# Kernel tuning notes

Measured on AMD Instinct MI355X. Metric: run time of the kernel, lower is better.

Reference implementation:

```python
import jax, jax.numpy as jnp
import numpy as np

N, C = 50000, 91
K_PRE = 1000            # pre-NMS top-k candidates (fixed shape for jit)
DET_PER_IMG = 100
SCORE_THRESH = 0.05
NMS_THRESH = 0.5
MIN_SIZE = 0.01
LOG_SCALE_CLAMP = float(np.log(1000.0 / 16.0))  # torchvision BoxCoder clamp
BBOX_W = (10.0, 10.0, 5.0, 5.0)


def setup_inputs() -> dict:
    key = jax.random.key(0)
    k1, k2, k3, k4, k5, k6 = jax.random.split(key, 6)
    class_logits = jax.random.normal(k1, (N, C), jnp.float32) * 2.0
    box_regression = jax.random.normal(k2, (N, C * 4), jnp.float32) * 0.5
    x1 = jax.random.uniform(k3, (N,), jnp.float32) * 1200.0
    y1 = jax.random.uniform(k4, (N,), jnp.float32) * 700.0
    w = jax.random.uniform(k5, (N,), jnp.float32) * 150.0 + 4.0
    h = jax.random.uniform(k6, (N,), jnp.float32) * 150.0 + 4.0
    proposals = jnp.stack([x1, y1, x1 + w, y1 + h], axis=1)
    return {"class_logits": class_logits, "box_regression": box_regression,
            "proposals": proposals, "image_h": 800, "image_w": 1333}


def _decode(rel, props):
    # torchvision BoxCoder.decode_single with weights (10,10,5,5)
    wx, wy, ww, wh = BBOX_W
    pw = props[:, 2] - props[:, 0]
    ph = props[:, 3] - props[:, 1]
    cx = props[:, 0] + 0.5 * pw
    cy = props[:, 1] + 0.5 * ph
    dx = rel[:, 0] / wx
    dy = rel[:, 1] / wy
    dw = jnp.minimum(rel[:, 2] / ww, LOG_SCALE_CLAMP)
    dh = jnp.minimum(rel[:, 3] / wh, LOG_SCALE_CLAMP)
    pcx = dx * pw + cx
    pcy = dy * ph + cy
    ppw = jnp.exp(dw) * pw
    pph = jnp.exp(dh) * ph
    return jnp.stack([pcx - 0.5 * ppw, pcy - 0.5 * pph,
                      pcx + 0.5 * ppw, pcy + 0.5 * pph], axis=1)


def _iou_matrix(b):
    # b: [K,4] -> [K,K] pairwise IoU
    area = jnp.maximum(b[:, 2] - b[:, 0], 0.0) * jnp.maximum(b[:, 3] - b[:, 1], 0.0)
    lt = jnp.maximum(b[:, None, :2], b[None, :, :2])
    rb = jnp.minimum(b[:, None, 2:], b[None, :, 2:])
    wh = jnp.maximum(rb - lt, 0.0)
    inter = wh[..., 0] * wh[..., 1]
    return inter / (area[:, None] + area[None, :] - inter + 1e-7)


def _postprocess(class_logits, box_regression, proposals, image_h, image_w):
    num_classes = class_logits.shape[-1]
    n = proposals.shape[0]
    props = jnp.broadcast_to(proposals[:, None, :], (n, num_classes, 4)).reshape(-1, 4)
    boxes = _decode(box_regression.reshape(-1, 4), props)       # [N*C, 4]
    # clip_boxes_to_image
    boxes = jnp.stack([
        jnp.clip(boxes[:, 0], 0.0, float(image_w)),
        jnp.clip(boxes[:, 1], 0.0, float(image_h)),
        jnp.clip(boxes[:, 2], 0.0, float(image_w)),
        jnp.clip(boxes[:, 3], 0.0, float(image_h)),
    ], axis=1)
    scores = jax.nn.softmax(class_logits, axis=-1)               # [N, C]
    # drop background class 0
    boxes = boxes.reshape(n, num_classes, 4)[:, 1:].reshape(-1, 4)    # [N*(C-1), 4]
    scores = scores[:, 1:].reshape(-1)                                # [N*(C-1)]
    labels = jnp.broadcast_to(jnp.arange(1, num_classes), (n, num_classes - 1)).reshape(-1)
    # score threshold + remove small boxes -> mask (fixed-shape)
    w = boxes[:, 2] - boxes[:, 0]
    h = boxes[:, 3] - boxes[:, 1]
    valid = (scores > SCORE_THRESH) & (w >= MIN_SIZE) & (h >= MIN_SIZE)
    masked_scores = jnp.where(valid, scores, -1.0)
    s_k, idx = jax.lax.top_k(masked_scores, K_PRE)               # pre-NMS candidates
    b_k = boxes[idx]
    l_k = labels[idx]
    keep0 = s_k > 0.0
    # batched NMS via per-class coordinate offset
    offset = l_k.astype(b_k.dtype) * float(image_w + image_h + 2)
    iou = _iou_matrix(b_k + offset[:, None])                     # [K,K]
    ar = jnp.arange(K_PRE)
    def body(i, keep):
        sup = keep[i] & (iou[i] > NMS_THRESH) & (ar > i)
        return keep & ~sup
    keep = jax.lax.fori_loop(0, K_PRE, body, keep0)
    final_scores = jnp.where(keep, s_k, -1.0)
    s_out, j = jax.lax.top_k(final_scores, DET_PER_IMG)
    ok = s_out > 0.0
    boxes_out = jnp.where(ok[:, None], b_k[j], 0.0)
    scores_out = jnp.where(ok, s_out, 0.0)
    labels_out = jnp.where(ok, l_k[j], 0)
    return boxes_out, scores_out, labels_out


def reference(class_logits, box_regression, proposals, image_h, image_w):
    return _postprocess(class_logits, box_regression, proposals, image_h, image_w)
```

## Files before the change

### kernel.cpp

```cpp
#include <hip/hip_runtime.h>
#include <cstdint>

#define NROWS 50000
#define NCLS  91
#define KPRE  1000
#define NDET  100
#define CAP   4096
#define NBINS 512
#define BIN_OFF 7680u
#define LOGCLAMP 4.135166556742356f
#define ROWS_PER_BLOCK 16
#define P1BLK 3125
#define GCHUNK 128

constexpr size_t OFF_CNT     = 0;
constexpr size_t OFF_ROWMAX  = 64;
constexpr size_t OFF_COMPACT = 100096;
constexpr size_t OFF_SSCORE  = 132864;
constexpr size_t OFF_SGIDX   = 136960;
constexpr size_t OFF_SLABEL  = 141056;
constexpr size_t OFF_BRAW    = 145152;
constexpr size_t OFF_BNMS    = 161536;
constexpr size_t OFF_MASK    = 177920;

__device__ __forceinline__ bool decode_box(int row, int c,
    const float* __restrict__ regr, const float* __restrict__ props,
    float W, float H, float4& b) {
  const float4 rr = *reinterpret_cast<const float4*>(regr + (size_t)row * (NCLS * 4) + c * 4);
  const float4 pp = *reinterpret_cast<const float4*>(props + (size_t)row * 4);
  float pw = pp.z - pp.x, ph = pp.w - pp.y;
  float cx = pp.x + 0.5f * pw, cy = pp.y + 0.5f * ph;
  float dx = rr.x / 10.0f, dy = rr.y / 10.0f;
  float dw = fminf(rr.z / 5.0f, LOGCLAMP);
  float dh = fminf(rr.w / 5.0f, LOGCLAMP);
  float pcx = dx * pw + cx, pcy = dy * ph + cy;
  float ppw = expf(dw) * pw, pph = expf(dh) * ph;
  float x1 = fminf(fmaxf(pcx - 0.5f * ppw, 0.f), W);
  float y1 = fminf(fmaxf(pcy - 0.5f * pph, 0.f), H);
  float x2 = fminf(fmaxf(pcx + 0.5f * ppw, 0.f), W);
  float y2 = fminf(fmaxf(pcy + 0.5f * pph, 0.f), H);
  b = make_float4(x1, y1, x2, y2);
  return (x2 - x1 >= 0.01f) && (y2 - y1 >= 0.01f);
}

__global__ __launch_bounds__(256)
void pass1_kernel(const float* __restrict__ logits,
                  const float* __restrict__ regr,
                  const float* __restrict__ props,
                  const int* __restrict__ p_imh,
                  const int* __restrict__ p_imw,
                  uint16_t* __restrict__ rowmax) {
  const int gt  = blockIdx.x * 256 + threadIdx.x;
  const int row = gt >> 4;
  const int sub = gt & 15;
  const float* lr = logits + (size_t)row * NCLS;

  float x[6];
  #pragma unroll
  for (int j = 0; j < 6; ++j) {
    int c = sub + 16 * j;
    x[j] = (c < NCLS) ? lr[c] : -INFINITY;
  }
  float m = x[0];
  #pragma unroll
  for (int j = 1; j < 6; ++j) m = fmaxf(m, x[j]);
  m = fmaxf(m, __shfl_xor(m, 1));
  m = fmaxf(m, __shfl_xor(m, 2));
  m = fmaxf(m, __shfl_xor(m, 4));
  m = fmaxf(m, __shfl_xor(m, 8));
  float e[6]; float s = 0.f;
  #pragma unroll
  for (int j = 0; j < 6; ++j) {
    e[j] = (sub + 16 * j < NCLS) ? expf(x[j] - m) : 0.f;
    s += e[j];
  }
  s += __shfl_xor(s, 1);
  s += __shfl_xor(s, 2);
  s += __shfl_xor(s, 4);
  s += __shfl_xor(s, 8);

  const float W = (float)(*p_imw), H = (float)(*p_imh);
  int maxbin = 0;
  #pragma unroll
  for (int j = 0; j < 6; ++j) {
    int c = sub + 16 * j;
    if (c >= 1 && c < NCLS) {
      float score = e[j] / s;
      if (score > 0.05f) {
        float4 b;
        if (decode_box(row, c, regr, props, W, H, b)) {
          uint32_t bin = (__float_as_uint(score) >> 17) - BIN_OFF;
          if ((int)bin > maxbin) maxbin = (int)bin;
        }
      }
    }
  }
  maxbin = max(maxbin, __shfl_xor(maxbin, 1));
  maxbin = max(maxbin, __shfl_xor(maxbin, 2));
  maxbin = max(maxbin, __shfl_xor(maxbin, 4));
  maxbin = max(maxbin, __shfl_xor(maxbin, 8));
  if (sub == 0) rowmax[row] = (uint16_t)maxbin;
}

__global__ __launch_bounds__(512)
void histscan_kernel(const uint16_t* __restrict__ rowmax, uint32_t* __restrict__ cnt) {
  __shared__ uint32_t sh[NBINS];
  const int t = threadIdx.x;
  sh[t] = 0;
  if (t == 0) cnt[1] = 0;
  __syncthreads();
  const uint32_t* r32 = reinterpret_cast<const uint32_t*>(rowmax);
  for (int k = t; k < NROWS / 2; k += 512) {
    uint32_t v = r32[k];
    uint32_t a = v & 0xffffu, b = v >> 16;
    if (a) atomicAdd(&sh[a], 1u);
    if (b) atomicAdd(&sh[b], 1u);
  }
  __syncthreads();
  uint32_t v = sh[t];
  for (int off = 1; off < NBINS; off <<= 1) {
    uint32_t add = (t + off < NBINS) ? sh[t + off] : 0;
    __syncthreads();
    v += add;
    sh[t] = v;
    __syncthreads();
  }
  const uint32_t total = sh[0];
  if (total == 0) { if (t == 0) cnt[0] = 0xFFFFFFFFu; return; }
  const uint32_t target = total < (uint32_t)KPRE ? total : (uint32_t)KPRE;
  const uint32_t rs_t = sh[t];
  const uint32_t rs_n = (t < NBINS - 1) ? sh[t + 1] : 0;
  if (rs_t >= target && rs_n < target) cnt[0] = (uint32_t)t;
}

__global__ __launch_bounds__(256)
void refine_kernel(const float* __restrict__ logits,
                   const float* __restrict__ regr,
                   const float* __restrict__ props,
                   const int* __restrict__ p_imh,
                   const int* __restrict__ p_imw,
                   const uint16_t* __restrict__ rowmax,
                   uint32_t* __restrict__ cnt,
                   unsigned long long* __restrict__ compact) {
  const int t = threadIdx.x;
  const int lane = t & 63;
  const int g = lane >> 4;
  const int sub = lane & 15;
  const uint32_t cut = cnt[0];
  const int myrow0 = blockIdx.x * 256 + t;
  bool qual = (myrow0 < NROWS) && ((uint32_t)rowmax[myrow0] >= cut);
  unsigned long long bm = __ballot(qual);
  if (!bm) return;
  const int waveBase = blockIdx.x * 256 + (t & ~63);
  const float W = (float)(*p_imw), H = (float)(*p_imh);

  while (bm) {
    int bsel[4];
    #pragma unroll
    for (int k = 0; k < 4; ++k) {
      bsel[k] = bm ? (__ffsll((unsigned long long)bm) - 1) : -1;
      if (bm) bm &= bm - 1;
    }
    const int myb = bsel[g];
    const int row = waveBase + (myb >= 0 ? myb : 0);
    const float* lr = logits + (size_t)row * NCLS;

    float x[6];
    #pragma unroll
    for (int j = 0; j < 6; ++j) {
      int c = sub + 16 * j;
      x[j] = (c < NCLS) ? lr[c] : -INFINITY;
    }
    float m = x[0];
    #pragma unroll
    for (int j = 1; j < 6; ++j) m = fmaxf(m, x[j]);
    m = fmaxf(m, __shfl_xor(m, 1));
    m = fmaxf(m, __shfl_xor(m, 2));
    m = fmaxf(m, __shfl_xor(m, 4));
    m = fmaxf(m, __shfl_xor(m, 8));
    float e[6]; float s = 0.f;
    #pragma unroll
    for (int j = 0; j < 6; ++j) {
      e[j] = (sub + 16 * j < NCLS) ? expf(x[j] - m) : 0.f;
      s += e[j];
    }
    s += __shfl_xor(s, 1);
    s += __shfl_xor(s, 2);
    s += __shfl_xor(s, 4);
    s += __shfl_xor(s, 8);

    if (myb >= 0) {
      #pragma unroll
      for (int j = 0; j < 6; ++j) {
        int c = sub + 16 * j;
        if (c >= 1 && c < NCLS) {
          float score = e[j] / s;
          if (score > 0.05f) {
            float4 bb;
            if (decode_box(row, c, regr, props, W, H, bb)) {
              uint32_t bits = __float_as_uint(score);
              uint32_t bin = (bits >> 17) - BIN_OFF;
              if (bin >= cut) {
                uint32_t pos = atomicAdd(&cnt[1], 1u);
                if (pos < CAP) {
                  uint32_t gidx = (uint32_t)row * 90u + (uint32_t)(c - 1);
                  compact[pos] = ((unsigned long long)bits << 32) |
                                 (unsigned long long)(0xFFFFFFFFu - gidx);
                }
              }
            }
          }
        }
      }
    }
  }
}

__global__ __launch_bounds__(1024)
void sort_prep_kernel(const unsigned long long* __restrict__ compact,
                      const uint32_t* __restrict__ cnt,
                      const float* __restrict__ regr, const float* __restrict__ props,
                      const int* __restrict__ p_imh, const int* __restrict__ p_imw,
                      float* __restrict__ sel_score, uint32_t* __restrict__ sel_gidx,
                      int* __restrict__ slabel, float4* __restrict__ braw,
                      float4* __restrict__ bnms) {
  __shared__ unsigned long long arr[CAP];
  const int t = threadIdx.x;
  const uint32_t M = cnt[1] < (uint32_t)CAP ? cnt[1] : (uint32_t)CAP;
  int P = 1024;
  while (P < (int)M) P <<= 1;
  for (int i = t; i < P; i += 1024) arr[i] = (i < (int)M) ? compact[i] : 0ull;
  __syncthreads();
  for (int k = 2; k <= P; k <<= 1) {
    for (int j = k >> 1; j > 0; j >>= 1) {
      for (int i = t; i < P; i += 1024) {
        int l = i ^ j;
        if (l > i) {
          unsigned long long A = arr[i], B = arr[l];
          bool up = ((i & k) == 0);
          if (up ? (A > B) : (A < B)) { arr[i] = B; arr[l] = A; }
        }
      }
      __syncthreads();
    }
  }
  if (t < KPRE) {
    unsigned long long en = arr[P - 1 - t];
    float sc; uint32_t g;
    if (en) { sc = __uint_as_float((uint32_t)(en >> 32)); g = 0xFFFFFFFFu - (uint32_t)en; }
    else    { sc = -1.f; g = 0xFFFFFFFFu; }
    sel_score[t] = sc;
    sel_gidx[t] = g;
    if (sc > 0.f) {
      int row = (int)(g / 90u);
      int c   = (int)(g % 90u) + 1;
      float W = (float)(*p_imw), H = (float)(*p_imh);
      float4 b;
      decode_box(row, c, regr, props, W, H, b);
      braw[t] = b;
      float offv = (float)c * (float)(*p_imw + *p_imh + 2);
      bnms[t] = make_float4(b.x + offv, b.y + offv, b.z + offv, b.w + offv);
      slabel[t] = c;
    } else {
      braw[t] = make_float4(0, 0, 0, 0);
      bnms[t] = make_float4(0, 0, 0, 0);
      slabel[t] = 0;
    }
  }
}

__global__ __launch_bounds__(256)
void iou_kernel(const float4* __restrict__ bnms, unsigned long long* __restrict__ mask) {
  const int i = blockIdx.x;
  const int lane = threadIdx.x & 63;
  const int wv = threadIdx.x >> 6;
  const float4 bi = bnms[i];
  const float areai = fmaxf(bi.z - bi.x, 0.f) * fmaxf(bi.w - bi.y, 0.f);
  #pragma unroll
  for (int ww = 0; ww < 4; ++ww) {
    int wd = wv * 4 + ww;
    int j = wd * 64 + lane;
    bool bit = false;
    if (j < KPRE && j > i) {
      float4 bj = bnms[j];
      float areaj = fmaxf(bj.z - bj.x, 0.f) * fmaxf(bj.w - bj.y, 0.f);
      float ltx = fmaxf(bi.x, bj.x), lty = fmaxf(bi.y, bj.y);
      float rbx = fminf(bi.z, bj.z), rby = fminf(bi.w, bj.w);
      float iw = fmaxf(rbx - ltx, 0.f), ih = fmaxf(rby - lty, 0.f);
      float inter = iw * ih;
      float iou = inter / (areai + areaj - inter + 1e-7f);
      bit = iou > 0.5f;
    }
    unsigned long long mword = __ballot(bit);
    if (lane == 0) mask[(size_t)i * 16 + wd] = mword;
  }
}

__global__ __launch_bounds__(256)
void greedy_kernel(const unsigned long long* __restrict__ mask,
                   const float* __restrict__ sel_score,
                   const int* __restrict__ slabel,
                   const float4* __restrict__ braw,
                   float* __restrict__ out) {
  __shared__ ulonglong2 buf[2][GCHUNK * 8];
  __shared__ int kept[NDET];
  __shared__ int s_done;
  const int t = threadIdx.x;
  const int lane = t & 63;
  const int wv = t >> 6;
  const ulonglong2* gm2 = reinterpret_cast<const ulonglong2*>(mask);
  constexpr int NCHUNK = (KPRE + GCHUNK - 1) / GCHUNK;

  unsigned long long kw = 0ull;
  #pragma unroll
  for (int w = 0; w < 16; ++w) {
    int j = w * 64 + lane;
    bool b = (j < KPRE) && (sel_score[j] > 0.f);
    unsigned long long mword = __ballot(b);
    if (lane == w) kw = mword;
  }
  if (t == 0) s_done = 0;

  {
    int rows = (KPRE < GCHUNK) ? KPRE : GCHUNK;
    int n2 = rows * 8;
    for (int k = t; k < n2; k += 256) buf[0][k] = gm2[k];
  }
  __syncthreads();

  int kc = 0;
  for (int c = 0; c < NCHUNK; ++c) {
    if (wv > 0 && c + 1 < NCHUNK) {
      int rows = KPRE - (c + 1) * GCHUNK;
      if (rows > GCHUNK) rows = GCHUNK;
      int n2 = rows * 8;
      size_t gbase = (size_t)(c + 1) * GCHUNK * 8;
      for (int k = t - 64; k < n2; k += 192) buf[(c + 1) & 1][k] = gm2[gbase + k];
    }
    if (wv == 0) {
      const unsigned long long* bb =
          reinterpret_cast<const unsigned long long*>(buf[c & 1]);
      int rows = KPRE - c * GCHUNK;
      if (rows > GCHUNK) rows = GCHUNK;
      unsigned long long curm = (lane < 16) ? bb[lane] : 0ull;
      for (int r = 0; r < rows; ++r) {
        unsigned long long nxt =
            (lane < 16 && r + 1 < rows) ? bb[(r + 1) * 16 + lane] : 0ull;
        int i = c * GCHUNK + r;
        unsigned long long kwv = __shfl(kw, i >> 6);
        if ((kwv >> (i & 63)) & 1ull) {
          if (lane == 0) kept[kc] = i;
          kw &= ~curm;
          ++kc;
          if (kc >= NDET) { if (lane == 0) s_done = 1; break; }
        }
        curm = nxt;
      }
    }
    __syncthreads();
    if (s_done) break;
  }

  if (wv == 0) {
    for (int q = lane; q < NDET; q += 64) {
      if (q < kc) {
        int i = kept[q];
        float4 b = braw[i];
        out[q * 4 + 0] = b.x; out[q * 4 + 1] = b.y;
        out[q * 4 + 2] = b.z; out[q * 4 + 3] = b.w;
        out[4 * NDET + q] = sel_score[i];
        out[5 * NDET + q] = (float)slabel[i];
      } else {
        out[q * 4 + 0] = 0.f; out[q * 4 + 1] = 0.f;
        out[q * 4 + 2] = 0.f; out[q * 4 + 3] = 0.f;
        out[4 * NDET + q] = 0.f;
        out[5 * NDET + q] = 0.f;
      }
    }
  }
}

extern "C" void kernel_launch(void* const* d_in, const int* in_sizes, int n_in,
                              void* d_out, int out_size, void* d_ws, size_t ws_size,
                              hipStream_t stream) {
  const float* logits = (const float*)d_in[0];
  const float* regr   = (const float*)d_in[1];
  const float* props  = (const float*)d_in[2];
  const int*   p_imh  = (const int*)d_in[3];
  const int*   p_imw  = (const int*)d_in[4];
  float* out = (float*)d_out;

  uint8_t* ws = (uint8_t*)d_ws;
  uint32_t* cnt  = (uint32_t*)(ws + OFF_CNT);
  uint16_t* rowmax = (uint16_t*)(ws + OFF_ROWMAX);
  unsigned long long* compact = (unsigned long long*)(ws + OFF_COMPACT);
  float*    sel_score = (float*)(ws + OFF_SSCORE);
  uint32_t* sel_gidx  = (uint32_t*)(ws + OFF_SGIDX);
  int*      slabel    = (int*)(ws + OFF_SLABEL);
  float4*   braw      = (float4*)(ws + OFF_BRAW);
  float4*   bnms      = (float4*)(ws + OFF_BNMS);
  unsigned long long* mask = (unsigned long long*)(ws + OFF_MASK);

  pass1_kernel<<<P1BLK, 256, 0, stream>>>(
      logits, regr, props, p_imh, p_imw, rowmax);
  histscan_kernel<<<1, NBINS, 0, stream>>>(rowmax, cnt);
  refine_kernel<<<(NROWS + 255) / 256, 256, 0, stream>>>(
      logits, regr, props, p_imh, p_imw, rowmax, cnt, compact);
  sort_prep_kernel<<<1, 1024, 0, stream>>>(compact, cnt, regr, props, p_imh, p_imw,
                                           sel_score, sel_gidx, slabel, braw, bnms);
  iou_kernel<<<KPRE, 256, 0, stream>>>(bnms, mask);
  greedy_kernel<<<1, 256, 0, stream>>>(mask, sel_score, slabel, braw, out);
}
```

Before: 101.0 us.

## Fuse pipeline into three kernels: redundant histogram in refine, single-block tail

Drops the separate histogram/scan kernel. Each of 49 refine blocks now rebuilds the score histogram redundantly in shared memory, using per-wave copies to cut atomic contention, and computes the cutoff itself. Sort, IoU mask, greedy NMS and output are merged into one 512-thread block that keeps boxes in registers and shared memory. Only the first 256 mask rows are precomputed; later suppression rows are computed on demand. This removes three launches and the global mask round-trip, at the cost of redundant histogram work per block, fewer refine blocks, and serialized IoU on one block.

```diff
diff --git a/kernel.cpp b/kernel.cpp
--- a/kernel.cpp
+++ b/kernel.cpp
@@ -9,19 +9,13 @@
 #define NBINS 512
 #define BIN_OFF 7680u
 #define LOGCLAMP 4.135166556742356f
-#define ROWS_PER_BLOCK 16
 #define P1BLK 3125
-#define GCHUNK 128
+#define R2BLK 49
+#define R2ROWS 1024
 
 constexpr size_t OFF_CNT     = 0;
 constexpr size_t OFF_ROWMAX  = 64;
 constexpr size_t OFF_COMPACT = 100096;
-constexpr size_t OFF_SSCORE  = 132864;
-constexpr size_t OFF_SGIDX   = 136960;
-constexpr size_t OFF_SLABEL  = 141056;
-constexpr size_t OFF_BRAW    = 145152;
-constexpr size_t OFF_BNMS    = 161536;
-constexpr size_t OFF_MASK    = 177920;
 
 __device__ __forceinline__ bool decode_box(int row, int c,
     const float* __restrict__ regr, const float* __restrict__ props,
@@ -49,7 +43,9 @@
                   const float* __restrict__ props,
                   const int* __restrict__ p_imh,
                   const int* __restrict__ p_imw,
-                  uint16_t* __restrict__ rowmax) {
+                  uint16_t* __restrict__ rowmax,
+                  uint32_t* __restrict__ cnt) {
+  if (blockIdx.x == 0 && threadIdx.x == 0) cnt[1] = 0;
   const int gt  = blockIdx.x * 256 + threadIdx.x;
   const int row = gt >> 4;
   const int sub = gt & 15;
@@ -102,37 +98,6 @@
   if (sub == 0) rowmax[row] = (uint16_t)maxbin;
 }
 
-__global__ __launch_bounds__(512)
-void histscan_kernel(const uint16_t* __restrict__ rowmax, uint32_t* __restrict__ cnt) {
-  __shared__ uint32_t sh[NBINS];
-  const int t = threadIdx.x;
-  sh[t] = 0;
-  if (t == 0) cnt[1] = 0;
-  __syncthreads();
-  const uint32_t* r32 = reinterpret_cast<const uint32_t*>(rowmax);
-  for (int k = t; k < NROWS / 2; k += 512) {
-    uint32_t v = r32[k];
-    uint32_t a = v & 0xffffu, b = v >> 16;
-    if (a) atomicAdd(&sh[a], 1u);
-    if (b) atomicAdd(&sh[b], 1u);
-  }
-  __syncthreads();
-  uint32_t v = sh[t];
-  for (int off = 1; off < NBINS; off <<= 1) {
-    uint32_t add = (t + off < NBINS) ? sh[t + off] : 0;
-    __syncthreads();
-    v += add;
-    sh[t] = v;
-    __syncthreads();
-  }
-  const uint32_t total = sh[0];
-  if (total == 0) { if (t == 0) cnt[0] = 0xFFFFFFFFu; return; }
-  const uint32_t target = total < (uint32_t)KPRE ? total : (uint32_t)KPRE;
-  const uint32_t rs_t = sh[t];
-  const uint32_t rs_n = (t < NBINS - 1) ? sh[t + 1] : 0;
-  if (rs_t >= target && rs_n < target) cnt[0] = (uint32_t)t;
-}
-
 __global__ __launch_bounds__(256)
 void refine_kernel(const float* __restrict__ logits,
                    const float* __restrict__ regr,
@@ -142,70 +107,111 @@
                    const uint16_t* __restrict__ rowmax,
                    uint32_t* __restrict__ cnt,
                    unsigned long long* __restrict__ compact) {
+  __shared__ uint32_t sh[4 * NBINS];
+  __shared__ uint32_t s_cut;
   const int t = threadIdx.x;
+  for (int k = t; k < 4 * NBINS; k += 256) sh[k] = 0;
+  __syncthreads();
+  const int wv4 = (t >> 6) * NBINS;
+  const uint32_t* r32 = reinterpret_cast<const uint32_t*>(rowmax);
+  for (int k = t; k < NROWS / 2; k += 256) {
+    uint32_t v = r32[k];
+    uint32_t a = v & 0xffffu, b = v >> 16;
+    if (a) atomicAdd(&sh[wv4 + a], 1u);
+    if (b) atomicAdd(&sh[wv4 + b], 1u);
+  }
+  __syncthreads();
+  uint32_t c0 = sh[t] + sh[NBINS + t] + sh[2 * NBINS + t] + sh[3 * NBINS + t];
+  uint32_t c1 = sh[256 + t] + sh[NBINS + 256 + t] + sh[2 * NBINS + 256 + t] +
+                sh[3 * NBINS + 256 + t];
+  __syncthreads();
+  sh[t] = c0; sh[256 + t] = c1;
+  __syncthreads();
+  for (int off = 1; off < NBINS; off <<= 1) {
+    uint32_t a0 = (t + off < NBINS) ? sh[t + off] : 0;
+    uint32_t a1 = (t + 256 + off < NBINS) ? sh[t + 256 + off] : 0;
+    __syncthreads();
+    sh[t] += a0;
+    sh[t + 256] += a1;
+    __syncthreads();
+  }
+  const uint32_t total = sh[0];
+  if (t == 0 && total == 0) s_cut = 0xFFFFFFFFu;
+  if (total != 0) {
+    const uint32_t target = total < (uint32_t)KPRE ? total : (uint32_t)KPRE;
+    #pragma unroll
+    for (int half = 0; half < 2; ++half) {
+      int b = t + half * 256;
+      uint32_t rs = sh[b];
+      uint32_t rsn = (b < NBINS - 1) ? sh[b + 1] : 0;
+      if (rs >= target && rsn < target) s_cut = (uint32_t)b;
+    }
+  }
+  __syncthreads();
+  const uint32_t cut = s_cut;
+
   const int lane = t & 63;
-  const int g = lane >> 4;
+  const int g16 = lane >> 4;
   const int sub = lane & 15;
-  const uint32_t cut = cnt[0];
-  const int myrow0 = blockIdx.x * 256 + t;
-  bool qual = (myrow0 < NROWS) && ((uint32_t)rowmax[myrow0] >= cut);
-  unsigned long long bm = __ballot(qual);
-  if (!bm) return;
-  const int waveBase = blockIdx.x * 256 + (t & ~63);
   const float W = (float)(*p_imw), H = (float)(*p_imh);
-
-  while (bm) {
-    int bsel[4];
-    #pragma unroll
-    for (int k = 0; k < 4; ++k) {
-      bsel[k] = bm ? (__ffsll((unsigned long long)bm) - 1) : -1;
-      if (bm) bm &= bm - 1;
-    }
-    const int myb = bsel[g];
-    const int row = waveBase + (myb >= 0 ? myb : 0);
-    const float* lr = logits + (size_t)row * NCLS;
-
-    float x[6];
-    #pragma unroll
-    for (int j = 0; j < 6; ++j) {
-      int c = sub + 16 * j;
-      x[j] = (c < NCLS) ? lr[c] : -INFINITY;
-    }
-    float m = x[0];
-    #pragma unroll
-    for (int j = 1; j < 6; ++j) m = fmaxf(m, x[j]);
-    m = fmaxf(m, __shfl_xor(m, 1));
-    m = fmaxf(m, __shfl_xor(m, 2));
-    m = fmaxf(m, __shfl_xor(m, 4));
-    m = fmaxf(m, __shfl_xor(m, 8));
-    float e[6]; float s = 0.f;
-    #pragma unroll
-    for (int j = 0; j < 6; ++j) {
-      e[j] = (sub + 16 * j < NCLS) ? expf(x[j] - m) : 0.f;
-      s += e[j];
-    }
-    s += __shfl_xor(s, 1);
-    s += __shfl_xor(s, 2);
-    s += __shfl_xor(s, 4);
-    s += __shfl_xor(s, 8);
-
-    if (myb >= 0) {
+  const int base = blockIdx.x * R2ROWS;
+  for (int pass = 0; pass < R2ROWS / 256; ++pass) {
+    const int myrow0 = base + pass * 256 + t;
+    bool qual = (myrow0 < NROWS) && ((uint32_t)rowmax[myrow0] >= cut);
+    unsigned long long bm = __ballot(qual);
+    if (!bm) continue;
+    const int waveBase = base + pass * 256 + (t & ~63);
+    while (bm) {
+      int bsel[4];
+      #pragma unroll
+      for (int k = 0; k < 4; ++k) {
+        bsel[k] = bm ? (__ffsll((unsigned long long)bm) - 1) : -1;
+        if (bm) bm &= bm - 1;
+      }
+      const int myb = bsel[g16];
+      const int row = waveBase + (myb >= 0 ? myb : 0);
+      const float* lr = logits + (size_t)row * NCLS;
+      float x[6];
       #pragma unroll
       for (int j = 0; j < 6; ++j) {
         int c = sub + 16 * j;
-        if (c >= 1 && c < NCLS) {
-          float score = e[j] / s;
-          if (score > 0.05f) {
-            float4 bb;
-            if (decode_box(row, c, regr, props, W, H, bb)) {
-              uint32_t bits = __float_as_uint(score);
-              uint32_t bin = (bits >> 17) - BIN_OFF;
-              if (bin >= cut) {
-                uint32_t pos = atomicAdd(&cnt[1], 1u);
-                if (pos < CAP) {
-                  uint32_t gidx = (uint32_t)row * 90u + (uint32_t)(c - 1);
-                  compact[pos] = ((unsigned long long)bits << 32) |
-                                 (unsigned long long)(0xFFFFFFFFu - gidx);
+        x[j] = (c < NCLS) ? lr[c] : -INFINITY;
+      }
+      float m = x[0];
+      #pragma unroll
+      for (int j = 1; j < 6; ++j) m = fmaxf(m, x[j]);
+      m = fmaxf(m, __shfl_xor(m, 1));
+      m = fmaxf(m, __shfl_xor(m, 2));
+      m = fmaxf(m, __shfl_xor(m, 4));
+      m = fmaxf(m, __shfl_xor(m, 8));
+      float e[6]; float s = 0.f;
+      #pragma unroll
+      for (int j = 0; j < 6; ++j) {
+        e[j] = (sub + 16 * j < NCLS) ? expf(x[j] - m) : 0.f;
+        s += e[j];
+      }
+      s += __shfl_xor(s, 1);
+      s += __shfl_xor(s, 2);
+      s += __shfl_xor(s, 4);
+      s += __shfl_xor(s, 8);
+      if (myb >= 0) {
+        #pragma unroll
+        for (int j = 0; j < 6; ++j) {
+          int c = sub + 16 * j;
+          if (c >= 1 && c < NCLS) {
+            float score = e[j] / s;
+            if (score > 0.05f) {
+              float4 bb;
+              if (decode_box(row, c, regr, props, W, H, bb)) {
+                uint32_t bits = __float_as_uint(score);
+                uint32_t bin = (bits >> 17) - BIN_OFF;
+                if (bin >= cut) {
+                  uint32_t pos = atomicAdd(&cnt[1], 1u);
+                  if (pos < CAP) {
+                    uint32_t gidx = (uint32_t)row * 90u + (uint32_t)(c - 1);
+                    compact[pos] = ((unsigned long long)bits << 32) |
+                                   (unsigned long long)(0xFFFFFFFFu - gidx);
+                  }
                 }
               }
             }
@@ -216,24 +222,45 @@
   }
 }
 
-__global__ __launch_bounds__(1024)
-void sort_prep_kernel(const unsigned long long* __restrict__ compact,
-                      const uint32_t* __restrict__ cnt,
-                      const float* __restrict__ regr, const float* __restrict__ props,
-                      const int* __restrict__ p_imh, const int* __restrict__ p_imw,
-                      float* __restrict__ sel_score, uint32_t* __restrict__ sel_gidx,
-                      int* __restrict__ slabel, float4* __restrict__ braw,
-                      float4* __restrict__ bnms) {
+__device__ __forceinline__ bool iou_gt(const float4& bi, float areai,
+                                       const float4& bj, float areaj) {
+  float ltx = fmaxf(bi.x, bj.x), lty = fmaxf(bi.y, bj.y);
+  float rbx = fminf(bi.z, bj.z), rby = fminf(bi.w, bj.w);
+  float iw = fmaxf(rbx - ltx, 0.f), ih = fmaxf(rby - lty, 0.f);
+  float inter = iw * ih;
+  float iou = inter / (areai + areaj - inter + 1e-7f);
+  return iou > 0.5f;
+}
+
+__global__ __launch_bounds__(512)
+void tail_kernel(const float* __restrict__ regr,
+                 const float* __restrict__ props,
+                 const int* __restrict__ p_imh,
+                 const int* __restrict__ p_imw,
+                 const uint32_t* __restrict__ cnt,
+                 const unsigned long long* __restrict__ compact,
+                 float* __restrict__ out) {
   __shared__ unsigned long long arr[CAP];
+  __shared__ float4 bnms_s[KPRE];
+  __shared__ float  score_s[KPRE];
+  __shared__ uint32_t gidx_s[KPRE];
+  __shared__ int kept[NDET];
+  __shared__ int s_kc;
   const int t = threadIdx.x;
-  const uint32_t M = cnt[1] < (uint32_t)CAP ? cnt[1] : (uint32_t)CAP;
+  const int lane = t & 63;
+  const int wv = t >> 6;
+  const float W = (float)(*p_imw), H = (float)(*p_imh);
+  const float offmul = (float)(*p_imw + *p_imh + 2);
+
+  const uint32_t Mc = cnt[1];
+  const uint32_t M = Mc < (uint32_t)CAP ? Mc : (uint32_t)CAP;
   int P = 1024;
   while (P < (int)M) P <<= 1;
-  for (int i = t; i < P; i += 1024) arr[i] = (i < (int)M) ? compact[i] : 0ull;
+  for (int i = t; i < P; i += 512) arr[i] = (i < (int)M) ? compact[i] : 0ull;
   __syncthreads();
   for (int k = 2; k <= P; k <<= 1) {
     for (int j = k >> 1; j > 0; j >>= 1) {
-      for (int i = t; i < P; i += 1024) {
+      for (int i = t; i < P; i += 512) {
         int l = i ^ j;
         if (l > i) {
           unsigned long long A = arr[i], B = arr[l];
@@ -244,138 +271,112 @@
       __syncthreads();
     }
   }
-  if (t < KPRE) {
-    unsigned long long en = arr[P - 1 - t];
-    float sc; uint32_t g;
-    if (en) { sc = __uint_as_float((uint32_t)(en >> 32)); g = 0xFFFFFFFFu - (uint32_t)en; }
-    else    { sc = -1.f; g = 0xFFFFFFFFu; }
-    sel_score[t] = sc;
-    sel_gidx[t] = g;
-    if (sc > 0.f) {
+  for (int q = t; q < KPRE; q += 512) {
+    unsigned long long en = arr[P - 1 - q];
+    if (en) {
+      float sc = __uint_as_float((uint32_t)(en >> 32));
+      uint32_t g = 0xFFFFFFFFu - (uint32_t)en;
+      score_s[q] = sc;
+      gidx_s[q] = g;
       int row = (int)(g / 90u);
       int c   = (int)(g % 90u) + 1;
-      float W = (float)(*p_imw), H = (float)(*p_imh);
       float4 b;
       decode_box(row, c, regr, props, W, H, b);
-      braw[t] = b;
-      float offv = (float)c * (float)(*p_imw + *p_imh + 2);
-      bnms[t] = make_float4(b.x + offv, b.y + offv, b.z + offv, b.w + offv);
-      slabel[t] = c;
+      float offv = (float)c * offmul;
+      bnms_s[q] = make_float4(b.x + offv, b.y + offv, b.z + offv, b.w + offv);
     } else {
-      braw[t] = make_float4(0, 0, 0, 0);
-      bnms[t] = make_float4(0, 0, 0, 0);
-      slabel[t] = 0;
-    }
-  }
-}
-
-__global__ __launch_bounds__(256)
-void iou_kernel(const float4* __restrict__ bnms, unsigned long long* __restrict__ mask) {
-  const int i = blockIdx.x;
-  const int lane = threadIdx.x & 63;
-  const int wv = threadIdx.x >> 6;
-  const float4 bi = bnms[i];
-  const float areai = fmaxf(bi.z - bi.x, 0.f) * fmaxf(bi.w - bi.y, 0.f);
-  #pragma unroll
-  for (int ww = 0; ww < 4; ++ww) {
-    int wd = wv * 4 + ww;
-    int j = wd * 64 + lane;
-    bool bit = false;
-    if (j < KPRE && j > i) {
-      float4 bj = bnms[j];
-      float areaj = fmaxf(bj.z - bj.x, 0.f) * fmaxf(bj.w - bj.y, 0.f);
-      float ltx = fmaxf(bi.x, bj.x), lty = fmaxf(bi.y, bj.y);
-      float rbx = fminf(bi.z, bj.z), rby = fminf(bi.w, bj.w);
-      float iw = fmaxf(rbx - ltx, 0.f), ih = fmaxf(rby - lty, 0.f);
-      float inter = iw * ih;
-      float iou = inter / (areai + areaj - inter + 1e-7f);
-      bit = iou > 0.5f;
-    }
-    unsigned long long mword = __ballot(bit);
-    if (lane == 0) mask[(size_t)i * 16 + wd] = mword;
-  }
-}
-
-__global__ __launch_bounds__(256)
-void greedy_kernel(const unsigned long long* __restrict__ mask,
-                   const float* __restrict__ sel_score,
-                   const int* __restrict__ slabel,
-                   const float4* __restrict__ braw,
-                   float* __restrict__ out) {
-  __shared__ ulonglong2 buf[2][GCHUNK * 8];
-  __shared__ int kept[NDET];
-  __shared__ int s_done;
-  const int t = threadIdx.x;
-  const int lane = t & 63;
-  const int wv = t >> 6;
-  const ulonglong2* gm2 = reinterpret_cast<const ulonglong2*>(mask);
-  constexpr int NCHUNK = (KPRE + GCHUNK - 1) / GCHUNK;
-
-  unsigned long long kw = 0ull;
+      score_s[q] = -1.f;
+      gidx_s[q] = 0xFFFFFFFFu;
+      bnms_s[q] = make_float4(0, 0, 0, 0);
+    }
+  }
+  __syncthreads();
+
+  float4 bj[16];
+  float  aj[16];
   #pragma unroll
   for (int w = 0; w < 16; ++w) {
     int j = w * 64 + lane;
-    bool b = (j < KPRE) && (sel_score[j] > 0.f);
-    unsigned long long mword = __ballot(b);
-    if (lane == w) kw = mword;
-  }
-  if (t == 0) s_done = 0;
-
-  {
-    int rows = (KPRE < GCHUNK) ? KPRE : GCHUNK;
-    int n2 = rows * 8;
-    for (int k = t; k < n2; k += 256) buf[0][k] = gm2[k];
-  }
-  __syncthreads();
-
-  int kc = 0;
-  for (int c = 0; c < NCHUNK; ++c) {
-    if (wv > 0 && c + 1 < NCHUNK) {
-      int rows = KPRE - (c + 1) * GCHUNK;
-      if (rows > GCHUNK) rows = GCHUNK;
-      int n2 = rows * 8;
-      size_t gbase = (size_t)(c + 1) * GCHUNK * 8;
-      for (int k = t - 64; k < n2; k += 192) buf[(c + 1) & 1][k] = gm2[gbase + k];
-    }
-    if (wv == 0) {
-      const unsigned long long* bb =
-          reinterpret_cast<const unsigned long long*>(buf[c & 1]);
-      int rows = KPRE - c * GCHUNK;
-      if (rows > GCHUNK) rows = GCHUNK;
-      unsigned long long curm = (lane < 16) ? bb[lane] : 0ull;
-      for (int r = 0; r < rows; ++r) {
-        unsigned long long nxt =
-            (lane < 16 && r + 1 < rows) ? bb[(r + 1) * 16 + lane] : 0ull;
-        int i = c * GCHUNK + r;
-        unsigned long long kwv = __shfl(kw, i >> 6);
-        if ((kwv >> (i & 63)) & 1ull) {
-          if (lane == 0) kept[kc] = i;
-          kw &= ~curm;
-          ++kc;
-          if (kc >= NDET) { if (lane == 0) s_done = 1; break; }
+    bj[w] = (j < KPRE) ? bnms_s[j] : make_float4(0, 0, 0, 0);
+    aj[w] = fmaxf(bj[w].z - bj[w].x, 0.f) * fmaxf(bj[w].w - bj[w].y, 0.f);
+  }
+  unsigned long long* mask256 = arr;
+  for (int i = wv; i < 256; i += 8) {
+    float4 bi = bnms_s[i];
+    float areai = fmaxf(bi.z - bi.x, 0.f) * fmaxf(bi.w - bi.y, 0.f);
+    unsigned long long myw = 0ull;
+    #pragma unroll
+    for (int w = 0; w < 16; ++w) {
+      int j = w * 64 + lane;
+      bool bit = (j < KPRE) && (j > i) && iou_gt(bi, areai, bj[w], aj[w]);
+      unsigned long long mword = __ballot(bit);
+      if (lane == w) myw = mword;
+    }
+    if (lane < 16) mask256[i * 16 + lane] = myw;
+  }
+  if (t == 0) s_kc = 0;
+  __syncthreads();
+
+  if (wv == 0) {
+    unsigned long long kw = 0ull;
+    #pragma unroll
+    for (int w = 0; w < 16; ++w) {
+      int j = w * 64 + lane;
+      bool b = (j < KPRE) && (score_s[j] > 0.f);
+      unsigned long long mword = __ballot(b);
+      if (lane == w) kw = mword;
+    }
+    int kc = 0;
+    int i = 0;
+    for (; i < 256 && kc < NDET; ++i) {
+      unsigned long long kwv = __shfl(kw, i >> 6);
+      if ((kwv >> (i & 63)) & 1ull) {
+        unsigned long long mrow = (lane < 16) ? mask256[i * 16 + lane] : 0ull;
+        if (lane == 0) kept[kc] = i;
+        kw &= ~mrow;
+        ++kc;
+      }
+    }
+    for (; i < KPRE && kc < NDET; ++i) {
+      unsigned long long kwv = __shfl(kw, i >> 6);
+      if ((kwv >> (i & 63)) & 1ull) {
+        if (lane == 0) kept[kc] = i;
+        float4 bi = bnms_s[i];
+        float areai = fmaxf(bi.z - bi.x, 0.f) * fmaxf(bi.w - bi.y, 0.f);
+        unsigned long long sup = 0ull;
+        #pragma unroll
+        for (int w = 0; w < 16; ++w) {
+          int j = w * 64 + lane;
+          bool bit = (j < KPRE) && (j > i) && iou_gt(bi, areai, bj[w], aj[w]);
+          unsigned long long mword = __ballot(bit);
+          if (lane == w) sup = mword;
         }
-        curm = nxt;
-      }
-    }
-    __syncthreads();
-    if (s_done) break;
-  }
-
-  if (wv == 0) {
-    for (int q = lane; q < NDET; q += 64) {
-      if (q < kc) {
-        int i = kept[q];
-        float4 b = braw[i];
-        out[q * 4 + 0] = b.x; out[q * 4 + 1] = b.y;
-        out[q * 4 + 2] = b.z; out[q * 4 + 3] = b.w;
-        out[4 * NDET + q] = sel_score[i];
-        out[5 * NDET + q] = (float)slabel[i];
-      } else {
-        out[q * 4 + 0] = 0.f; out[q * 4 + 1] = 0.f;
-        out[q * 4 + 2] = 0.f; out[q * 4 + 3] = 0.f;
-        out[4 * NDET + q] = 0.f;
-        out[5 * NDET + q] = 0.f;
-      }
+        kw &= ~sup;
+        ++kc;
+      }
+    }
+    if (lane == 0) s_kc = kc;
+  }
+  __syncthreads();
+
+  const int kc = s_kc;
+  for (int q = t; q < NDET; q += 512) {
+    if (q < kc) {
+      int i = kept[q];
+      uint32_t g = gidx_s[i];
+      int row = (int)(g / 90u);
+      int c   = (int)(g % 90u) + 1;
+      float4 b;
+      decode_box(row, c, regr, props, W, H, b);
+      out[q * 4 + 0] = b.x; out[q * 4 + 1] = b.y;
+      out[q * 4 + 2] = b.z; out[q * 4 + 3] = b.w;
+      out[4 * NDET + q] = score_s[i];
+      out[5 * NDET + q] = (float)c;
+    } else {
+      out[q * 4 + 0] = 0.f; out[q * 4 + 1] = 0.f;
+      out[q * 4 + 2] = 0.f; out[q * 4 + 3] = 0.f;
+      out[4 * NDET + q] = 0.f;
+      out[5 * NDET + q] = 0.f;
     }
   }
 }
@@ -394,20 +395,11 @@
   uint32_t* cnt  = (uint32_t*)(ws + OFF_CNT);
   uint16_t* rowmax = (uint16_t*)(ws + OFF_ROWMAX);
   unsigned long long* compact = (unsigned long long*)(ws + OFF_COMPACT);
-  float*    sel_score = (float*)(ws + OFF_SSCORE);
-  uint32_t* sel_gidx  = (uint32_t*)(ws + OFF_SGIDX);
-  int*      slabel    = (int*)(ws + OFF_SLABEL);
-  float4*   braw      = (float4*)(ws + OFF_BRAW);
-  float4*   bnms      = (float4*)(ws + OFF_BNMS);
-  unsigned long long* mask = (unsigned long long*)(ws + OFF_MASK);
 
   pass1_kernel<<<P1BLK, 256, 0, stream>>>(
-      logits, regr, props, p_imh, p_imw, rowmax);
-  histscan_kernel<<<1, NBINS, 0, stream>>>(rowmax, cnt);
-  refine_kernel<<<(NROWS + 255) / 256, 256, 0, stream>>>(
+      logits, regr, props, p_imh, p_imw, rowmax, cnt);
+  refine_kernel<<<R2BLK, 256, 0, stream>>>(
       logits, regr, props, p_imh, p_imw, rowmax, cnt, compact);
-  sort_prep_kernel<<<1, 1024, 0, stream>>>(compact, cnt, regr, props, p_imh, p_imw,
-                                           sel_score, sel_gidx, slabel, braw, bnms);
-  iou_kernel<<<KPRE, 256, 0, stream>>>(bnms, mask);
-  greedy_kernel<<<1, 256, 0, stream>>>(mask, sel_score, slabel, braw, out);
-}
+  tail_kernel<<<1, 512, 0, stream>>>(
+      regr, props, p_imh, p_imw, cnt, compact, out);
+}
```

After: 168.8 us. 1.67x slower.

## Fuse histogram scan into refine kernel with finer bins and fewer blocks

Applied to the files above, without the earlier changes.

Drops the separate single-block histogram/scan kernel. Each of 49 refine blocks now builds the row-max histogram itself in shared memory and computes the score cutoff before gathering candidates, which removes one launch and its serial dependency. Score bins go from 512 to 2304 (shift 14 instead of 17), so the cutoff is finer and fewer extra candidates pass it. The cost is that every block redundantly reads all 50k rowmax entries and runs a block scan, and each block now covers 1024 rows, so there are fewer blocks for the gather.

```diff
diff --git a/kernel.cpp b/kernel.cpp
--- a/kernel.cpp
+++ b/kernel.cpp
@@ -6,11 +6,13 @@
 #define KPRE  1000
 #define NDET  100
 #define CAP   4096
-#define NBINS 512
-#define BIN_OFF 7680u
+#define NBINS 2304
+#define BIN_OFF 62770u
 #define LOGCLAMP 4.135166556742356f
-#define ROWS_PER_BLOCK 16
 #define P1BLK 3125
+#define R2BLK 49
+#define R2ROWS 1024
+#define BPT 9
 #define GCHUNK 128
 
 constexpr size_t OFF_CNT     = 0;
@@ -49,7 +51,9 @@
                   const float* __restrict__ props,
                   const int* __restrict__ p_imh,
                   const int* __restrict__ p_imw,
-                  uint16_t* __restrict__ rowmax) {
+                  uint16_t* __restrict__ rowmax,
+                  uint32_t* __restrict__ cnt) {
+  if (blockIdx.x == 0 && threadIdx.x == 0) cnt[1] = 0;
   const int gt  = blockIdx.x * 256 + threadIdx.x;
   const int row = gt >> 4;
   const int sub = gt & 15;
@@ -89,7 +93,7 @@
       if (score > 0.05f) {
         float4 b;
         if (decode_box(row, c, regr, props, W, H, b)) {
-          uint32_t bin = (__float_as_uint(score) >> 17) - BIN_OFF;
+          uint32_t bin = (__float_as_uint(score) >> 14) - BIN_OFF;
           if ((int)bin > maxbin) maxbin = (int)bin;
         }
       }
@@ -100,37 +104,6 @@
   maxbin = max(maxbin, __shfl_xor(maxbin, 4));
   maxbin = max(maxbin, __shfl_xor(maxbin, 8));
   if (sub == 0) rowmax[row] = (uint16_t)maxbin;
-}
-
-__global__ __launch_bounds__(512)
-void histscan_kernel(const uint16_t* __restrict__ rowmax, uint32_t* __restrict__ cnt) {
-  __shared__ uint32_t sh[NBINS];
-  const int t = threadIdx.x;
-  sh[t] = 0;
-  if (t == 0) cnt[1] = 0;
-  __syncthreads();
-  const uint32_t* r32 = reinterpret_cast<const uint32_t*>(rowmax);
-  for (int k = t; k < NROWS / 2; k += 512) {
-    uint32_t v = r32[k];
-    uint32_t a = v & 0xffffu, b = v >> 16;
-    if (a) atomicAdd(&sh[a], 1u);
-    if (b) atomicAdd(&sh[b], 1u);
-  }
-  __syncthreads();
-  uint32_t v = sh[t];
-  for (int off = 1; off < NBINS; off <<= 1) {
-    uint32_t add = (t + off < NBINS) ? sh[t + off] : 0;
-    __syncthreads();
-    v += add;
-    sh[t] = v;
-    __syncthreads();
-  }
-  const uint32_t total = sh[0];
-  if (total == 0) { if (t == 0) cnt[0] = 0xFFFFFFFFu; return; }
-  const uint32_t target = total < (uint32_t)KPRE ? total : (uint32_t)KPRE;
-  const uint32_t rs_t = sh[t];
-  const uint32_t rs_n = (t < NBINS - 1) ? sh[t + 1] : 0;
-  if (rs_t >= target && rs_n < target) cnt[0] = (uint32_t)t;
 }
 
 __global__ __launch_bounds__(256)
@@ -142,70 +115,118 @@
                    const uint16_t* __restrict__ rowmax,
                    uint32_t* __restrict__ cnt,
                    unsigned long long* __restrict__ compact) {
+  __shared__ uint32_t sh[2 * NBINS];
+  __shared__ uint32_t csum[256 + 1];
+  __shared__ uint32_t s_cut;
   const int t = threadIdx.x;
+  for (int k = t; k < 2 * NBINS; k += 256) sh[k] = 0;
+  if (t == 0) { csum[256] = 0; s_cut = 0xFFFFFFFFu; }
+  __syncthreads();
+  const int sb = (t >> 7) * NBINS;
+  const uint32_t* r32 = reinterpret_cast<const uint32_t*>(rowmax);
+  for (int k = t; k < NROWS / 2; k += 256) {
+    uint32_t v = r32[k];
+    uint32_t a = v & 0xffffu, b = v >> 16;
+    if (a) atomicAdd(&sh[sb + a], 1u);
+    if (b) atomicAdd(&sh[sb + b], 1u);
+  }
+  __syncthreads();
+  uint32_t mysum = 0;
+  uint32_t hloc[BPT];
+  #pragma unroll
+  for (int q = 0; q < BPT; ++q) {
+    int b = t * BPT + q;
+    uint32_t hv = sh[b] + sh[NBINS + b];
+    hloc[q] = hv;
+    mysum += hv;
+  }
+  csum[t] = mysum;
+  __syncthreads();
+  uint32_t v = mysum;
+  for (int off = 1; off < 256; off <<= 1) {
+    uint32_t add = (t + off < 256) ? csum[t + off] : 0;
+    __syncthreads();
+    v += add;
+    csum[t] = v;
+    __syncthreads();
+  }
+  const uint32_t total = csum[0];
+  if (total != 0) {
+    const uint32_t target = total < (uint32_t)KPRE ? total : (uint32_t)KPRE;
+    const uint32_t sfx_next = (t < 255) ? csum[t + 1] : 0;
+    if (csum[t] >= target && sfx_next < target) {
+      uint32_t acc = sfx_next;
+      for (int q = BPT - 1; q >= 0; --q) {
+        acc += hloc[q];
+        if (acc >= target) { s_cut = (uint32_t)(t * BPT + q); break; }
+      }
+    }
+  }
+  __syncthreads();
+  const uint32_t cut = s_cut;
+
   const int lane = t & 63;
-  const int g = lane >> 4;
+  const int g16 = lane >> 4;
   const int sub = lane & 15;
-  const uint32_t cut = cnt[0];
-  const int myrow0 = blockIdx.x * 256 + t;
-  bool qual = (myrow0 < NROWS) && ((uint32_t)rowmax[myrow0] >= cut);
-  unsigned long long bm = __ballot(qual);
-  if (!bm) return;
-  const int waveBase = blockIdx.x * 256 + (t & ~63);
   const float W = (float)(*p_imw), H = (float)(*p_imh);
-
-  while (bm) {
-    int bsel[4];
-    #pragma unroll
-    for (int k = 0; k < 4; ++k) {
-      bsel[k] = bm ? (__ffsll((unsigned long long)bm) - 1) : -1;
-      if (bm) bm &= bm - 1;
-    }
-    const int myb = bsel[g];
-    const int row = waveBase + (myb >= 0 ? myb : 0);
-    const float* lr = logits + (size_t)row * NCLS;
-
-    float x[6];
-    #pragma unroll
-    for (int j = 0; j < 6; ++j) {
-      int c = sub + 16 * j;
-      x[j] = (c < NCLS) ? lr[c] : -INFINITY;
-    }
-    float m = x[0];
-    #pragma unroll
-    for (int j = 1; j < 6; ++j) m = fmaxf(m, x[j]);
-    m = fmaxf(m, __shfl_xor(m, 1));
-    m = fmaxf(m, __shfl_xor(m, 2));
-    m = fmaxf(m, __shfl_xor(m, 4));
-    m = fmaxf(m, __shfl_xor(m, 8));
-    float e[6]; float s = 0.f;
-    #pragma unroll
-    for (int j = 0; j < 6; ++j) {
-      e[j] = (sub + 16 * j < NCLS) ? expf(x[j] - m) : 0.f;
-      s += e[j];
-    }
-    s += __shfl_xor(s, 1);
-    s += __shfl_xor(s, 2);
-    s += __shfl_xor(s, 4);
-    s += __shfl_xor(s, 8);
-
-    if (myb >= 0) {
+  const int base = blockIdx.x * R2ROWS;
+  for (int pass = 0; pass < R2ROWS / 256; ++pass) {
+    const int myrow0 = base + pass * 256 + t;
+    bool qual = (myrow0 < NROWS) && ((uint32_t)rowmax[myrow0] >= cut);
+    unsigned long long bm = __ballot(qual);
+    if (!bm) continue;
+    const int waveBase = base + pass * 256 + (t & ~63);
+    while (bm) {
+      int bsel[4];
+      #pragma unroll
+      for (int k = 0; k < 4; ++k) {
+        bsel[k] = bm ? (__ffsll((unsigned long long)bm) - 1) : -1;
+        if (bm) bm &= bm - 1;
+      }
+      const int myb = bsel[g16];
+      const int row = waveBase + (myb >= 0 ? myb : 0);
+      const float* lr = logits + (size_t)row * NCLS;
+      float x[6];
       #pragma unroll
       for (int j = 0; j < 6; ++j) {
         int c = sub + 16 * j;
-        if (c >= 1 && c < NCLS) {
-          float score = e[j] / s;
-          if (score > 0.05f) {
-            float4 bb;
-            if (decode_box(row, c, regr, props, W, H, bb)) {
-              uint32_t bits = __float_as_uint(score);
-              uint32_t bin = (bits >> 17) - BIN_OFF;
-              if (bin >= cut) {
-                uint32_t pos = atomicAdd(&cnt[1], 1u);
-                if (pos < CAP) {
-                  uint32_t gidx = (uint32_t)row * 90u + (uint32_t)(c - 1);
-                  compact[pos] = ((unsigned long long)bits << 32) |
-                                 (unsigned long long)(0xFFFFFFFFu - gidx);
+        x[j] = (c < NCLS) ? lr[c] : -INFINITY;
+      }
+      float m = x[0];
+      #pragma unroll
+      for (int j = 1; j < 6; ++j) m = fmaxf(m, x[j]);
+      m = fmaxf(m, __shfl_xor(m, 1));
+      m = fmaxf(m, __shfl_xor(m, 2));
+      m = fmaxf(m, __shfl_xor(m, 4));
+      m = fmaxf(m, __shfl_xor(m, 8));
+      float e[6]; float s = 0.f;
+      #pragma unroll
+      for (int j = 0; j < 6; ++j) {
+        e[j] = (sub + 16 * j < NCLS) ? expf(x[j] - m) : 0.f;
+        s += e[j];
+      }
+      s += __shfl_xor(s, 1);
+      s += __shfl_xor(s, 2);
+      s += __shfl_xor(s, 4);
+      s += __shfl_xor(s, 8);
+      if (myb >= 0) {
+        #pragma unroll
+        for (int j = 0; j < 6; ++j) {
+          int c = sub + 16 * j;
+          if (c >= 1 && c < NCLS) {
+            float score = e[j] / s;
+            if (score > 0.05f) {
+              float4 bb;
+              if (decode_box(row, c, regr, props, W, H, bb)) {
+                uint32_t bits = __float_as_uint(score);
+                uint32_t bin = (bits >> 14) - BIN_OFF;
+                if (bin >= cut) {
+                  uint32_t pos = atomicAdd(&cnt[1], 1u);
+                  if (pos < CAP) {
+                    uint32_t gidx = (uint32_t)row * 90u + (uint32_t)(c - 1);
+                    compact[pos] = ((unsigned long long)bits << 32) |
+                                   (unsigned long long)(0xFFFFFFFFu - gidx);
+                  }
                 }
               }
             }
@@ -402,9 +423,8 @@
   unsigned long long* mask = (unsigned long long*)(ws + OFF_MASK);
 
   pass1_kernel<<<P1BLK, 256, 0, stream>>>(
-      logits, regr, props, p_imh, p_imw, rowmax);
-  histscan_kernel<<<1, NBINS, 0, stream>>>(rowmax, cnt);
-  refine_kernel<<<(NROWS + 255) / 256, 256, 0, stream>>>(
+      logits, regr, props, p_imh, p_imw, rowmax, cnt);
+  refine_kernel<<<R2BLK, 256, 0, stream>>>(
       logits, regr, props, p_imh, p_imw, rowmax, cnt, compact);
   sort_prep_kernel<<<1, 1024, 0, stream>>>(compact, cnt, regr, props, p_imh, p_imw,
                                            sel_score, sel_gidx, slabel, braw, bnms);
```

New measurement: 118.2 us. 17.0% more time.
